# Performance work log

Measured on AMD Instinct MI355X. Metric: run time of the kernel, lower is better.

The kernel has to match this reference:

```python
import jax, jax.numpy as jnp
import numpy as np


def _blended_linear(h, W, b, blend):
    # Equivalent to building w[b] = sum_e blend[e,b]*W[e] (shape B,out,in)
    # and computing w[b] @ h[b] + sum_e blend[e,b]*b[e], without the huge
    # per-sample weight tensor.
    # h: (B, in), W: (E, out, in), b: (E, out), blend: (E, B) -> (B, out)
    y = jnp.einsum('eoi,bi->ebo', W, h)          # per-expert outputs
    y = jnp.einsum('eb,ebo->bo', blend, y)       # blend across experts
    return y + blend.T @ b                       # blended bias


def setup_inputs() -> dict:
    key = jax.random.key(0)
    ks = jax.random.split(key, 9)
    E, B = 8, 8192
    dims = [480, 512, 512, 363]
    inp = {
        'x': jax.random.normal(ks[0], (B, dims[0]), jnp.float32),
        'weight_blend': jax.random.uniform(ks[1], (E, B), jnp.float32),
        'W1': jax.random.normal(ks[2], (E, dims[1], dims[0]), jnp.float32) * 0.05,
        'b1': jax.random.normal(ks[3], (E, dims[1]), jnp.float32) * 0.05,
        'W2': jax.random.normal(ks[4], (E, dims[2], dims[1]), jnp.float32) * 0.05,
        'b2': jax.random.normal(ks[5], (E, dims[2]), jnp.float32) * 0.05,
        'W3': jax.random.normal(ks[6], (E, dims[3], dims[2]), jnp.float32) * 0.05,
        'b3': jax.random.normal(ks[7], (E, dims[3]), jnp.float32) * 0.05,
        'batch_size': B,
    }
    return inp


def reference(x, weight_blend, W1, b1, W2, b2, W3, b3, batch_size):
    # Dropout layers are identity in eval mode; final_ac=True -> softmax.
    h = _blended_linear(x, W1, b1, weight_blend)
    h = jax.nn.elu(h)
    h = _blended_linear(h, W2, b2, weight_blend)
    h = jax.nn.elu(h)
    h = _blended_linear(h, W3, b3, weight_blend)
    return jax.nn.softmax(h, axis=-1)
```

## Files before the change

### kernel.cpp

```cpp
#include <hip/hip_runtime.h>
#include <cstdint>

#define E_EXP 8
#define BATCH 8192
#define D0 480
#define D1 512
#define D2 512
#define D3 363
#define KP 512
#define N3PAD 384

typedef _Float16 f16x8 __attribute__((ext_vector_type(8)));
typedef float f32x4 __attribute__((ext_vector_type(4)));
typedef unsigned short u16;
typedef u16 u16x8 __attribute__((ext_vector_type(8)));

__device__ __forceinline__ u16 f2h(float f) {
    _Float16 h = (_Float16)f;
    return __builtin_bit_cast(u16, h);
}

__device__ __forceinline__ void async16(const u16* g, u16* s) {
    __builtin_amdgcn_global_load_lds(
        reinterpret_cast<const __attribute__((address_space(1))) void*>(
            reinterpret_cast<uintptr_t>(g)),
        reinterpret_cast<__attribute__((address_space(3))) void*>(
            reinterpret_cast<uintptr_t>(s)),
        16, 0, 0);
}

__device__ __forceinline__ void pack_seg(const float* __restrict__ src,
                                         u16* __restrict__ dst,
                                         int OUT_src, int OUTP, int IN_src) {
    int total = E_EXP * OUTP * 128;
    int in4 = IN_src >> 2;
    for (int idx = blockIdx.x * blockDim.x + threadIdx.x; idx < total;
         idx += gridDim.x * blockDim.x) {
        int e = idx / (OUTP * 128);
        int r = idx - e * OUTP * 128;
        int o = r >> 7;
        int k4 = r & 127;
        ushort4 w;
        if (o < OUT_src && k4 < in4) {
            const float4 v = *reinterpret_cast<const float4*>(
                src + ((size_t)e * OUT_src + o) * IN_src + (k4 << 2));
            w.x = f2h(v.x); w.y = f2h(v.y); w.z = f2h(v.z); w.w = f2h(v.w);
        } else {
            w.x = 0; w.y = 0; w.z = 0; w.w = 0;
        }
        *reinterpret_cast<ushort4*>(dst + ((size_t)e * OUTP + o) * KP + (k4 << 2)) = w;
    }
}

__global__ void pack_all(const float* __restrict__ W1, const float* __restrict__ W2,
                         const float* __restrict__ W3, u16* __restrict__ wf1,
                         u16* __restrict__ wf2, u16* __restrict__ wf3) {
    pack_seg(W1, wf1, 512, 512, D0);
    pack_seg(W2, wf2, 512, 512, D1);
    pack_seg(W3, wf3, D3, N3PAD, D2);
}

__global__ void pad_x(const float* __restrict__ x, u16* __restrict__ xp) {
    int total = BATCH * 128;
    for (int idx = blockIdx.x * blockDim.x + threadIdx.x; idx < total;
         idx += gridDim.x * blockDim.x) {
        int b = idx >> 7, k4 = idx & 127;
        ushort4 w;
        if (k4 < 120) {
            const float4 v = *reinterpret_cast<const float4*>(
                x + (size_t)b * D0 + (k4 << 2));
            w.x = f2h(v.x); w.y = f2h(v.y); w.z = f2h(v.z); w.w = f2h(v.w);
        } else {
            w.x = 0; w.y = 0; w.z = 0; w.w = 0;
        }
        *reinterpret_cast<ushort4*>(xp + (size_t)b * KP + (k4 << 2)) = w;
    }
}

__global__ __launch_bounds__(512, 2) void gemm_all(
    const u16* __restrict__ A, const u16* __restrict__ Bw,
    const float* __restrict__ blend, const float* __restrict__ bias,
    u16* __restrict__ out, int OUTP, int OUTR, int nbn, int mode) {
    __shared__ __align__(16) u16 As[16384];
    __shared__ __align__(16) u16 Bs[32768];
    const int tid = threadIdx.x;
    const int w = tid >> 6, lane = tid & 63;
    const int wm2 = w & 3, wn2 = w >> 2;
    const int q = lane >> 4, l15 = lane & 15;

    const int id = blockIdx.x;
    const int xcd = id & 7;
    const int j = id >> 3;
    const int bm = ((j & 3) << 3) + xcd;
    const int bn = j >> 2;

    f32x4 acc[4][2];
#pragma unroll
    for (int mi = 0; mi < 4; ++mi)
#pragma unroll
        for (int ni = 0; ni < 2; ++ni) acc[mi][ni] = (f32x4){0.f, 0.f, 0.f, 0.f};

    _Float16 blh[8][4];
#pragma unroll
    for (int e = 0; e < 8; ++e)
#pragma unroll
        for (int mi = 0; mi < 4; ++mi)
            blh[e][mi] = (_Float16)blend[e * BATCH + bm * 256 + wm2 * 64 +
                                         mi * 16 + l15];

    const int l8 = lane & 7, h8 = lane >> 3;
    const int c8 = (l8 ^ h8) << 3;
    const size_t EST = (size_t)OUTP * KP;
    const u16* gA = A + (size_t)(bm * 256 + w * 32 + h8) * KP + c8;
    const u16* gB = Bw + (size_t)w * EST + (size_t)(bn * 64 + h8) * KP + c8;
    u16* sA = As + w * 2048;
    u16* sB = Bs + w * 4096;

    for (int kt = 0; kt < 8; ++kt) {
        const int ko = kt * 64;
#pragma unroll
        for (int u = 0; u < 4; ++u)
            async16(gA + (size_t)u * 8 * KP + ko, sA + u * 512);
#pragma unroll
        for (int u = 0; u < 8; ++u)
            async16(gB + (size_t)u * 8 * KP + ko, sB + u * 512);
        __syncthreads();
#pragma unroll
        for (int ks = 0; ks < 2; ++ks) {
            const int cs = (((q ^ (l15 & 7)) << 3) ^ (ks << 5));
            f16x8 af[4];
#pragma unroll
            for (int mi = 0; mi < 4; ++mi)
                af[mi] = *reinterpret_cast<const f16x8*>(
                    &As[(wm2 * 64 + mi * 16 + l15) * 64 + cs]);
#pragma unroll
            for (int e = 0; e < 8; ++e) {
                f16x8 bf0 = *reinterpret_cast<const f16x8*>(
                    &Bs[e * 4096 + (wn2 * 32 + l15) * 64 + cs]);
                f16x8 bf1 = *reinterpret_cast<const f16x8*>(
                    &Bs[e * 4096 + (wn2 * 32 + 16 + l15) * 64 + cs]);
#pragma unroll
                for (int mi = 0; mi < 4; ++mi) {
                    f16x8 as = af[mi] * blh[e][mi];
                    acc[mi][0] = __builtin_amdgcn_mfma_f32_16x16x32_f16(
                        as, bf0, acc[mi][0], 0, 0, 0);
                    acc[mi][1] = __builtin_amdgcn_mfma_f32_16x16x32_f16(
                        as, bf1, acc[mi][1], 0, 0, 0);
                }
            }
        }
        __syncthreads();
    }

    float* Blf = reinterpret_cast<float*>(As);
    float* Bif = reinterpret_cast<float*>(Bs);
    for (int idx = tid; idx < 2048; idx += 512) {
        int e = idx >> 8, r = idx & 255;
        Blf[r * 8 + e] = blend[e * BATCH + bm * 256 + r];
    }
    {
        int e = tid >> 6, c = tid & 63;
        int cg = bn * 64 + c;
        Bif[c * 8 + e] = (cg < OUTR) ? bias[e * OUTR + cg] : 0.f;
    }
    __syncthreads();
#pragma unroll
    for (int mi = 0; mi < 4; ++mi) {
#pragma unroll
        for (int ni = 0; ni < 2; ++ni) {
            int col_l = wn2 * 32 + ni * 16 + l15;
            int gcol = bn * 64 + col_l;
#pragma unroll
            for (int r = 0; r < 4; ++r) {
                int rl = wm2 * 64 + mi * 16 + q * 4 + r;
                float bb = 0.f;
#pragma unroll
                for (int e = 0; e < 8; ++e)
                    bb += Blf[rl * 8 + e] * Bif[col_l * 8 + e];
                float v = acc[mi][ni][r] + bb;
                if (mode == 0) v = v > 0.f ? v : expm1f(v);
                out[(size_t)(bm * 256 + rl) * OUTP + gcol] = f2h(v);
            }
        }
    }
}

__global__ __launch_bounds__(128) void softmax_rows(
    const u16* __restrict__ P, float* __restrict__ out) {
    const int b = blockIdx.x;
    const int tid = threadIdx.x, lane = tid & 63, w = tid >> 6;
    float v[3];
    int n = 0;
    float mx = -3.4e38f;
    for (int i = tid; i < D3; i += 128) {
        float s = (float)*reinterpret_cast<const _Float16*>(
            P + (size_t)b * N3PAD + i);
        v[n] = s; mx = fmaxf(mx, s); ++n;
    }
#pragma unroll
    for (int off = 32; off >= 1; off >>= 1) mx = fmaxf(mx, __shfl_xor(mx, off, 64));
    __shared__ float sm[4];
    if (lane == 0) sm[w] = mx;
    __syncthreads();
    mx = fmaxf(sm[0], sm[1]);
    float s = 0.f;
    for (int jj = 0; jj < n; ++jj) { v[jj] = expf(v[jj] - mx); s += v[jj]; }
#pragma unroll
    for (int off = 32; off >= 1; off >>= 1) s += __shfl_xor(s, off, 64);
    if (lane == 0) sm[2 + w] = s;
    __syncthreads();
    float inv = 1.f / (sm[2] + sm[3]);
    n = 0;
    for (int i = tid; i < D3; i += 128) { out[(size_t)b * D3 + i] = v[n] * inv; ++n; }
}

extern "C" void kernel_launch(void* const* d_in, const int* in_sizes, int n_in,
                              void* d_out, int out_size, void* d_ws, size_t ws_size,
                              hipStream_t stream) {
    const float* x = (const float*)d_in[0];
    const float* blend = (const float*)d_in[1];
    const float* W1 = (const float*)d_in[2];
    const float* b1 = (const float*)d_in[3];
    const float* W2 = (const float*)d_in[4];
    const float* b2 = (const float*)d_in[5];
    const float* W3 = (const float*)d_in[6];
    const float* b3 = (const float*)d_in[7];
    float* outp = (float*)d_out;

    char* ws = (char*)d_ws;
    u16* wf1 = (u16*)ws; ws += (size_t)E_EXP * 512 * KP * 2;
    u16* wf2 = (u16*)ws; ws += (size_t)E_EXP * 512 * KP * 2;
    u16* wf3 = (u16*)ws; ws += (size_t)E_EXP * N3PAD * KP * 2;
    u16* xp = (u16*)ws;  ws += (size_t)BATCH * KP * 2;
    u16* h1 = (u16*)ws;  ws += (size_t)BATCH * KP * 2;
    u16* h2 = (u16*)ws;  ws += (size_t)BATCH * KP * 2;
    u16* P = (u16*)ws;

    pack_all<<<1024, 256, 0, stream>>>(W1, W2, W3, wf1, wf2, wf3);
    pad_x<<<2048, 256, 0, stream>>>(x, xp);

    gemm_all<<<32 * 8, 512, 0, stream>>>(xp, wf1, blend, b1, h1, 512, 512, 8, 0);
    gemm_all<<<32 * 8, 512, 0, stream>>>(h1, wf2, blend, b2, h2, 512, 512, 8, 0);
    gemm_all<<<32 * 6, 512, 0, stream>>>(h2, wf3, blend, b3, P, N3PAD, D3, 6, 1);
    softmax_rows<<<BATCH, 128, 0, stream>>>(P, outp);
}
```

Before: 220.2 us.

## Double-buffer GEMM K-tiles in LDS to overlap async loads with MFMA

The K loop now steps through 32-wide tiles instead of 64-wide ones and keeps two LDS buffers. The async global-to-LDS loads for the next tile are issued before the MFMAs run on the current tile, with one barrier per iteration instead of two. The LDS swizzle is reworked for the 32-element row stride. The intent is to hide global load latency behind compute, at the cost of more loop iterations and barriers. LDS footprint stays at 96KB, so occupancy is unchanged.

```diff
diff --git a/kernel.cpp b/kernel.cpp
--- a/kernel.cpp
+++ b/kernel.cpp
@@ -81,8 +81,7 @@
     const u16* __restrict__ A, const u16* __restrict__ Bw,
     const float* __restrict__ blend, const float* __restrict__ bias,
     u16* __restrict__ out, int OUTP, int OUTR, int nbn, int mode) {
-    __shared__ __align__(16) u16 As[16384];
-    __shared__ __align__(16) u16 Bs[32768];
+    __shared__ __align__(16) u16 S[49152];
     const int tid = threadIdx.x;
     const int w = tid >> 6, lane = tid & 63;
     const int wm2 = w & 3, wn2 = w >> 2;
@@ -108,52 +107,66 @@
             blh[e][mi] = (_Float16)blend[e * BATCH + bm * 256 + wm2 * 64 +
                                          mi * 16 + l15];
 
-    const int l8 = lane & 7, h8 = lane >> 3;
-    const int c8 = (l8 ^ h8) << 3;
+    const int l4r = lane >> 2;
+    const int l4s = lane & 3;
+    const int ks8 = (l4s ^ (l4r & 3)) << 3;
     const size_t EST = (size_t)OUTP * KP;
-    const u16* gA = A + (size_t)(bm * 256 + w * 32 + h8) * KP + c8;
-    const u16* gB = Bw + (size_t)w * EST + (size_t)(bn * 64 + h8) * KP + c8;
-    u16* sA = As + w * 2048;
-    u16* sB = Bs + w * 4096;
-
-    for (int kt = 0; kt < 8; ++kt) {
-        const int ko = kt * 64;
-#pragma unroll
-        for (int u = 0; u < 4; ++u)
-            async16(gA + (size_t)u * 8 * KP + ko, sA + u * 512);
-#pragma unroll
-        for (int u = 0; u < 8; ++u)
-            async16(gB + (size_t)u * 8 * KP + ko, sB + u * 512);
+    const u16* gA0 = A + (size_t)(bm * 256 + w * 32 + l4r) * KP + ks8;
+    const u16* gB0 = Bw + (size_t)w * EST + (size_t)(bn * 64 + l4r) * KP + ks8;
+    const size_t R16 = (size_t)16 * KP;
+    const int aBase = w * 1024;
+    const int bBase = 8192 + w * 2048;
+
+    const int ra = (q ^ (l15 & 3)) << 3;
+    const int arow[4] = {(wm2 * 64 + 0 * 16 + l15) * 32 + ra,
+                         (wm2 * 64 + 1 * 16 + l15) * 32 + ra,
+                         (wm2 * 64 + 2 * 16 + l15) * 32 + ra,
+                         (wm2 * 64 + 3 * 16 + l15) * 32 + ra};
+    const int brow0 = (wn2 * 32 + l15) * 32 + ra;
+    const int brow1 = (wn2 * 32 + 16 + l15) * 32 + ra;
+
+    auto stage = [&](int kt, int p) {
+        const int ko = kt << 5;
+        u16* buf = S + p * 24576;
+        async16(gA0 + ko, buf + aBase);
+        async16(gA0 + R16 + ko, buf + aBase + 512);
+        async16(gB0 + ko, buf + bBase);
+        async16(gB0 + R16 + ko, buf + bBase + 512);
+        async16(gB0 + 2 * R16 + ko, buf + bBase + 1024);
+        async16(gB0 + 3 * R16 + ko, buf + bBase + 1536);
+    };
+
+    stage(0, 0);
+    __syncthreads();
+
+#pragma unroll 2
+    for (int kt = 0; kt < 16; ++kt) {
+        const int p = kt & 1;
+        if (kt < 15) stage(kt + 1, p ^ 1);
+        const u16* As_ = S + p * 24576;
+        const u16* Bs_ = As_ + 8192;
+        f16x8 af[4];
+#pragma unroll
+        for (int mi = 0; mi < 4; ++mi)
+            af[mi] = *reinterpret_cast<const f16x8*>(&As_[arow[mi]]);
+#pragma unroll
+        for (int e = 0; e < 8; ++e) {
+            f16x8 bf0 = *reinterpret_cast<const f16x8*>(&Bs_[e * 2048 + brow0]);
+            f16x8 bf1 = *reinterpret_cast<const f16x8*>(&Bs_[e * 2048 + brow1]);
+#pragma unroll
+            for (int mi = 0; mi < 4; ++mi) {
+                f16x8 as = af[mi] * blh[e][mi];
+                acc[mi][0] = __builtin_amdgcn_mfma_f32_16x16x32_f16(
+                    as, bf0, acc[mi][0], 0, 0, 0);
+                acc[mi][1] = __builtin_amdgcn_mfma_f32_16x16x32_f16(
+                    as, bf1, acc[mi][1], 0, 0, 0);
+            }
+        }
         __syncthreads();
-#pragma unroll
-        for (int ks = 0; ks < 2; ++ks) {
-            const int cs = (((q ^ (l15 & 7)) << 3) ^ (ks << 5));
-            f16x8 af[4];
-#pragma unroll
-            for (int mi = 0; mi < 4; ++mi)
-                af[mi] = *reinterpret_cast<const f16x8*>(
-                    &As[(wm2 * 64 + mi * 16 + l15) * 64 + cs]);
-#pragma unroll
-            for (int e = 0; e < 8; ++e) {
-                f16x8 bf0 = *reinterpret_cast<const f16x8*>(
-                    &Bs[e * 4096 + (wn2 * 32 + l15) * 64 + cs]);
-                f16x8 bf1 = *reinterpret_cast<const f16x8*>(
-                    &Bs[e * 4096 + (wn2 * 32 + 16 + l15) * 64 + cs]);
-#pragma unroll
-                for (int mi = 0; mi < 4; ++mi) {
-                    f16x8 as = af[mi] * blh[e][mi];
-                    acc[mi][0] = __builtin_amdgcn_mfma_f32_16x16x32_f16(
-                        as, bf0, acc[mi][0], 0, 0, 0);
-                    acc[mi][1] = __builtin_amdgcn_mfma_f32_16x16x32_f16(
-                        as, bf1, acc[mi][1], 0, 0, 0);
-                }
-            }
-        }
-        __syncthreads();
-    }
-
-    float* Blf = reinterpret_cast<float*>(As);
-    float* Bif = reinterpret_cast<float*>(Bs);
+    }
+
+    float* Blf = reinterpret_cast<float*>(S);
+    float* Bif = reinterpret_cast<float*>(S + 16384);
     for (int idx = tid; idx < 2048; idx += 512) {
         int e = idx >> 8, r = idx & 255;
         Blf[r * 8 + e] = blend[e * BATCH + bm * 256 + r];
```

Result: faster. 212.1 us (-3.7%).
